# Kernel optimization log

Measured on AMD Instinct MI355X. Metric: run time of the kernel, lower is better.

## Reference

```python
import jax, jax.numpy as jnp
import numpy as np

N_NODES = 100000
N_EDGES = 800000
D_IN, D_H1, D_H2, D_OUT = 512, 256, 256, 64


def setup_inputs() -> dict:
    key = jax.random.key(0)
    ks = jax.random.split(key, 8)
    x = jax.random.normal(ks[0], (N_NODES, D_IN), dtype=jnp.float32)
    edge_index = jax.random.randint(ks[1], (2, N_EDGES), 0, N_NODES, dtype=jnp.int64)
    # Glorot-style scaled weights (PyG GCNConv uses glorot init; Linear uses kaiming-uniform).
    W1 = jax.random.normal(ks[2], (D_IN, D_H1), dtype=jnp.float32) / np.sqrt(D_IN)
    b1 = jnp.zeros((D_H1,), dtype=jnp.float32)
    W2 = jax.random.normal(ks[3], (D_H1, D_H2), dtype=jnp.float32) / np.sqrt(D_H1)
    b2 = jnp.zeros((D_H2,), dtype=jnp.float32)
    Wc = jax.random.normal(ks[4], (D_H2, D_OUT), dtype=jnp.float32) / np.sqrt(D_H2)
    bc = jnp.zeros((D_OUT,), dtype=jnp.float32)
    return {"x": x, "edge_index": edge_index, "W1": W1, "b1": b1,
            "W2": W2, "b2": b2, "Wc": Wc, "bc": bc}


def reference(x, edge_index, W1, b1, W2, b2, Wc, bc):
    # GCNModel.forward in eval mode (dropout is identity when training=False).
    N = x.shape[0]
    src, dst = edge_index[0], edge_index[1]
    # PyG GCNConv: add self-loops, symmetric normalization D^-1/2 (A+I) D^-1/2.
    deg = jnp.zeros((N,), x.dtype).at[dst].add(jnp.float32(1.0)) + 1.0  # in-degree + self-loop
    dinv = jax.lax.rsqrt(deg)                         # [N]
    norm = dinv[src] * dinv[dst]                      # [E] per-edge coefficient
    self_norm = (dinv * dinv)[:, None]                # [N,1] self-loop coefficient 1/deg

    def gcn_conv(h, W, b):
        h = h @ W                                     # transform first (PyG order)
        agg = jax.ops.segment_sum(h[src] * norm[:, None], dst, num_segments=N)
        return agg + h * self_norm + b

    h = jax.nn.relu(gcn_conv(x, W1, b1))
    h = jax.nn.relu(gcn_conv(h, W2, b2))
    return h @ Wc + bc                                # [N, num_classes]
```

## Files before the change

### kernel.cpp

```cpp
#include <hip/hip_runtime.h>
#include <cstdint>

#define DIN 512
#define DH  256
#define DOUT 64

typedef __attribute__((ext_vector_type(8))) short bf16x8;
typedef __attribute__((ext_vector_type(4))) float f32x4;
typedef unsigned int uint32;

__device__ __forceinline__ unsigned short f2bf(float f) {
    uint32 u = __float_as_uint(f);
    u += 0x7fff + ((u >> 16) & 1);
    return (unsigned short)(u >> 16);
}
__device__ __forceinline__ float bf2f(unsigned short h) {
    return __uint_as_float(((uint32)h) << 16);
}
__device__ __forceinline__ float bflo(uint32 u) { return __uint_as_float(u << 16); }
__device__ __forceinline__ float bfhi(uint32 u) { return __uint_as_float(u & 0xffff0000u); }

__global__ void detect_i64(const unsigned long long* ei, int n_check,
                           unsigned long long bound, int* flag) {
    __shared__ int ok;
    if (threadIdx.x == 0) ok = 1;
    __syncthreads();
    int bad = 0;
    for (int i = threadIdx.x; i < n_check; i += blockDim.x) {
        if (ei[i] >= bound) bad = 1;
    }
    if (bad) ok = 0;
    __syncthreads();
    if (threadIdx.x == 0) *flag = ok;
}

__device__ __forceinline__ int get_idx(const void* ei, int is64, int pos) {
    if (is64) return (int)((const long long*)ei)[pos];
    return ((const int*)ei)[pos];
}

__global__ void count_deg(const void* ei, const int* flag, int E, int* counts) {
    const int is64 = *flag;
    int e = blockIdx.x * blockDim.x + threadIdx.x;
    if (e >= E) return;
    int d = get_idx(ei, is64, E + e);
    atomicAdd(&counts[d], 1);
}

__global__ void compute_dinv(const int* counts, float* dinv, int N) {
    int i = blockIdx.x * blockDim.x + threadIdx.x;
    if (i < N) dinv[i] = rsqrtf((float)counts[i] + 1.0f);
}

#define SCAN_BLOCK 256
#define SCAN_ELEMS 1024

__global__ void scan1(const int* counts, int* out, int* blocksums, int N) {
    __shared__ int sh[SCAN_BLOCK];
    int base = blockIdx.x * SCAN_ELEMS;
    int t = threadIdx.x;
    int v[4];
    int s = 0;
    #pragma unroll
    for (int j = 0; j < 4; j++) {
        int idx = base + t * 4 + j;
        v[j] = (idx < N) ? counts[idx] : 0;
        s += v[j];
    }
    sh[t] = s;
    __syncthreads();
    for (int off = 1; off < SCAN_BLOCK; off <<= 1) {
        int x = (t >= off) ? sh[t - off] : 0;
        __syncthreads();
        sh[t] += x;
        __syncthreads();
    }
    int run = (t == 0) ? 0 : sh[t - 1];
    #pragma unroll
    for (int j = 0; j < 4; j++) {
        int idx = base + t * 4 + j;
        if (idx < N) out[idx] = run;
        run += v[j];
    }
    if (t == SCAN_BLOCK - 1) blocksums[blockIdx.x] = sh[t];
}

__global__ void scan2(int* blocksums, int NB) {
    __shared__ int sh[SCAN_BLOCK];
    int t = threadIdx.x;
    sh[t] = (t < NB) ? blocksums[t] : 0;
    __syncthreads();
    for (int off = 1; off < SCAN_BLOCK; off <<= 1) {
        int x = (t >= off) ? sh[t - off] : 0;
        __syncthreads();
        sh[t] += x;
        __syncthreads();
    }
    if (t < NB) blocksums[t] = (t == 0) ? 0 : sh[t - 1];
}

__global__ void scan3(int* row_ptr, const int* blocksums, int N, int E) {
    int i = blockIdx.x * blockDim.x + threadIdx.x;
    if (i < N) row_ptr[i] += blocksums[i / SCAN_ELEMS];
    if (i == N) row_ptr[N] = E;
}

__global__ void fill_csr(const void* ei, const int* flag, int E,
                         const int* row_ptr, int* cursor, int* col_idx,
                         const float* dinv, float* edge_w) {
    const int is64 = *flag;
    int e = blockIdx.x * blockDim.x + threadIdx.x;
    if (e >= E) return;
    int d = get_idx(ei, is64, E + e);
    int s = get_idx(ei, is64, e);
    int pos = row_ptr[d] + atomicAdd(&cursor[d], 1);
    col_idx[pos] = s;
    edge_w[pos] = dinv[s] * dinv[d];
}

__global__ void transpose_w(const float* __restrict__ W, unsigned short* __restrict__ Bt,
                            int K, int Nw) {
    int i = blockIdx.x * blockDim.x + threadIdx.x;
    if (i >= K * Nw) return;
    int k = i / Nw, n = i % Nw;
    Bt[(size_t)n * K + k] = f2bf(W[i]);
}

template <bool A_FP32>
__global__ __launch_bounds__(512) void gemm_mfma(const void* __restrict__ Ap,
                                                 const unsigned short* __restrict__ Bt,
                                                 unsigned short* __restrict__ C,
                                                 int M, int K) {
    __shared__ unsigned short lds[24576];
    unsigned short* As = lds;
    unsigned short* Bs = lds + 8192;
    const int tid = threadIdx.x;
    const int w = tid >> 6, l = tid & 63;
    const int m0 = blockIdx.x * 128;
    const int wr = w >> 2, wc = w & 3;

    f32x4 acc[4][4] = {};

    for (int k0 = 0; k0 < K; k0 += 64) {
        #pragma unroll
        for (int i = 0; i < 4; i++) {
            int row = i * 64 + (tid >> 3);
            const unsigned short* src = Bt + (size_t)row * K + k0 + (tid & 7) * 8;
            unsigned short* dst = Bs + row * 64 + (tid & 7) * 8;
            __builtin_amdgcn_global_load_lds(
                (const __attribute__((address_space(1))) uint32*)src,
                (__attribute__((address_space(3))) uint32*)dst, 16, 0, 0);
        }
        if (A_FP32) {
            const float* Af = (const float*)Ap;
            #pragma unroll
            for (int i = 0; i < 4; i++) {
                int row = i * 32 + (tid >> 4);
                int rg = m0 + row; if (rg > M - 1) rg = M - 1;
                int c4 = (tid & 15) * 4;
                float4 v = *(const float4*)(Af + (size_t)rg * K + k0 + c4);
                ushort4 h;
                h.x = f2bf(v.x); h.y = f2bf(v.y); h.z = f2bf(v.z); h.w = f2bf(v.w);
                *(ushort4*)(As + row * 64 + c4) = h;
            }
        } else {
            const unsigned short* Ab = (const unsigned short*)Ap;
            #pragma unroll
            for (int i = 0; i < 2; i++) {
                int row = i * 64 + (tid >> 3);
                int rg = m0 + row; if (rg > M - 1) rg = M - 1;
                const unsigned short* src = Ab + (size_t)rg * K + k0 + (tid & 7) * 8;
                unsigned short* dst = As + row * 64 + (tid & 7) * 8;
                __builtin_amdgcn_global_load_lds(
                    (const __attribute__((address_space(1))) uint32*)src,
                    (__attribute__((address_space(3))) uint32*)dst, 16, 0, 0);
            }
        }
        __syncthreads();
        #pragma unroll
        for (int ks = 0; ks < 2; ks++) {
            bf16x8 a[4], b[4];
            #pragma unroll
            for (int m = 0; m < 4; m++)
                a[m] = *(const bf16x8*)(As + (wr * 64 + m * 16 + (l & 15)) * 64 + ks * 32 + (l >> 4) * 8);
            #pragma unroll
            for (int n = 0; n < 4; n++)
                b[n] = *(const bf16x8*)(Bs + (wc * 64 + n * 16 + (l & 15)) * 64 + ks * 32 + (l >> 4) * 8);
            #pragma unroll
            for (int m = 0; m < 4; m++)
                #pragma unroll
                for (int n = 0; n < 4; n++)
                    acc[m][n] = __builtin_amdgcn_mfma_f32_16x16x32_bf16(a[m], b[n], acc[m][n], 0, 0, 0);
        }
        __syncthreads();
    }

    unsigned short* ep = lds + (w & 3) * 4096;
    #pragma unroll
    for (int ph = 0; ph < 2; ph++) {
        if ((w >> 2) == ph) {
            #pragma unroll
            for (int m = 0; m < 4; m++)
                #pragma unroll
                for (int n = 0; n < 4; n++)
                    #pragma unroll
                    for (int r = 0; r < 4; r++)
                        ep[(m * 16 + (l >> 4) * 4 + r) * 64 + n * 16 + (l & 15)] = f2bf(acc[m][n][r]);
        }
        __syncthreads();
        if ((w >> 2) == ph) {
            #pragma unroll
            for (int p = 0; p < 8; p++) {
                int row = p * 8 + (l >> 3);
                int gr = m0 + wr * 64 + row;
                uint4 v = *(const uint4*)(ep + row * 64 + (l & 7) * 8);
                if (gr < M)
                    *(uint4*)(C + (size_t)gr * 256 + wc * 64 + (l & 7) * 8) = v;
            }
        }
        __syncthreads();
    }
}

__global__ __launch_bounds__(256) void gemm_head(const unsigned short* __restrict__ A,
                                                 const unsigned short* __restrict__ Bt,
                                                 const float* __restrict__ bias,
                                                 float* __restrict__ out, int M) {
    __shared__ unsigned short As[128 * 64];
    __shared__ unsigned short Bs[64 * 64];
    const int tid = threadIdx.x;
    const int w = tid >> 6, l = tid & 63;
    const int m0 = blockIdx.x * 128;
    const int wr = w >> 1, wc = w & 1;
    f32x4 acc[4][2] = {};

    for (int k0 = 0; k0 < 256; k0 += 64) {
        #pragma unroll
        for (int i = 0; i < 4; i++) {
            int row = i * 32 + w * 8 + (l >> 3);
            int rg = m0 + row; if (rg > M - 1) rg = M - 1;
            __builtin_amdgcn_global_load_lds(
                (const __attribute__((address_space(1))) uint32*)(A + (size_t)rg * 256 + k0 + (l & 7) * 8),
                (__attribute__((address_space(3))) uint32*)(As + row * 64 + (l & 7) * 8), 16, 0, 0);
        }
        #pragma unroll
        for (int i = 0; i < 2; i++) {
            int row = i * 32 + w * 8 + (l >> 3);
            __builtin_amdgcn_global_load_lds(
                (const __attribute__((address_space(1))) uint32*)(Bt + (size_t)row * 256 + k0 + (l & 7) * 8),
                (__attribute__((address_space(3))) uint32*)(Bs + row * 64 + (l & 7) * 8), 16, 0, 0);
        }
        __syncthreads();
        #pragma unroll
        for (int ks = 0; ks < 2; ks++) {
            bf16x8 a[4], b[2];
            #pragma unroll
            for (int m = 0; m < 4; m++)
                a[m] = *(const bf16x8*)(As + (wr * 64 + m * 16 + (l & 15)) * 64 + ks * 32 + (l >> 4) * 8);
            #pragma unroll
            for (int n = 0; n < 2; n++)
                b[n] = *(const bf16x8*)(Bs + (wc * 32 + n * 16 + (l & 15)) * 64 + ks * 32 + (l >> 4) * 8);
            #pragma unroll
            for (int m = 0; m < 4; m++)
                #pragma unroll
                for (int n = 0; n < 2; n++)
                    acc[m][n] = __builtin_amdgcn_mfma_f32_16x16x32_bf16(a[m], b[n], acc[m][n], 0, 0, 0);
        }
        __syncthreads();
    }
    #pragma unroll
    for (int m = 0; m < 4; m++)
        #pragma unroll
        for (int n = 0; n < 2; n++)
            #pragma unroll
            for (int r = 0; r < 4; r++) {
                int gr = m0 + wr * 64 + m * 16 + (l >> 4) * 4 + r;
                int col = wc * 32 + n * 16 + (l & 15);
                if (gr < M) out[(size_t)gr * 64 + col] = acc[m][n][r] + bias[col];
            }
}

#define ACC8(v, wgt)                                    \
    do {                                                \
        acc[0] = fmaf(wgt, bflo(v.x), acc[0]);          \
        acc[1] = fmaf(wgt, bfhi(v.x), acc[1]);          \
        acc[2] = fmaf(wgt, bflo(v.y), acc[2]);          \
        acc[3] = fmaf(wgt, bfhi(v.y), acc[3]);          \
        acc[4] = fmaf(wgt, bflo(v.z), acc[4]);          \
        acc[5] = fmaf(wgt, bfhi(v.z), acc[5]);          \
        acc[6] = fmaf(wgt, bflo(v.w), acc[6]);          \
        acc[7] = fmaf(wgt, bfhi(v.w), acc[7]);          \
    } while (0)

__global__ __launch_bounds__(256) void aggregate_bf(const unsigned short* __restrict__ t,
                                                    const float* __restrict__ dinv,
                                                    const int* __restrict__ row_ptr,
                                                    const int* __restrict__ col_idx,
                                                    const float* __restrict__ edge_w,
                                                    const float* __restrict__ bias,
                                                    unsigned short* __restrict__ outb,
                                                    int N) {
    int wave = threadIdx.x >> 6;
    int lane = threadIdx.x & 63;
    int half = lane >> 5;
    int sl = lane & 31;
    int n = blockIdx.x * 8 + wave * 2 + half;
    if (n >= N) return;

    float dn = dinv[n];
    int r0 = row_ptr[n], r1 = row_ptr[n + 1];

    float acc[8];
    {
        uint4 sv = *(const uint4*)(t + (size_t)n * DH + sl * 8);
        float sn = dn * dn;
        acc[0] = bflo(sv.x) * sn; acc[1] = bfhi(sv.x) * sn;
        acc[2] = bflo(sv.y) * sn; acc[3] = bfhi(sv.y) * sn;
        acc[4] = bflo(sv.z) * sn; acc[5] = bfhi(sv.z) * sn;
        acc[6] = bflo(sv.w) * sn; acc[7] = bfhi(sv.w) * sn;
    }

    int j = r0;
    for (; j + 4 <= r1; j += 4) {
        int s0 = col_idx[j + 0], s1 = col_idx[j + 1];
        int s2 = col_idx[j + 2], s3 = col_idx[j + 3];
        float w0 = edge_w[j + 0], w1 = edge_w[j + 1];
        float w2 = edge_w[j + 2], w3 = edge_w[j + 3];
        uint4 v0 = *(const uint4*)(t + (size_t)s0 * DH + sl * 8);
        uint4 v1 = *(const uint4*)(t + (size_t)s1 * DH + sl * 8);
        uint4 v2 = *(const uint4*)(t + (size_t)s2 * DH + sl * 8);
        uint4 v3 = *(const uint4*)(t + (size_t)s3 * DH + sl * 8);
        ACC8(v0, w0); ACC8(v1, w1); ACC8(v2, w2); ACC8(v3, w3);
    }
    for (; j < r1; j++) {
        int s = col_idx[j];
        float wgt = edge_w[j];
        uint4 v = *(const uint4*)(t + (size_t)s * DH + sl * 8);
        ACC8(v, wgt);
    }

    float4 b0 = *(const float4*)(bias + sl * 8);
    float4 b1v = *(const float4*)(bias + sl * 8 + 4);
    acc[0] = fmaxf(acc[0] + b0.x, 0.f);  acc[1] = fmaxf(acc[1] + b0.y, 0.f);
    acc[2] = fmaxf(acc[2] + b0.z, 0.f);  acc[3] = fmaxf(acc[3] + b0.w, 0.f);
    acc[4] = fmaxf(acc[4] + b1v.x, 0.f); acc[5] = fmaxf(acc[5] + b1v.y, 0.f);
    acc[6] = fmaxf(acc[6] + b1v.z, 0.f); acc[7] = fmaxf(acc[7] + b1v.w, 0.f);

    uint4 o;
    o.x = (uint32)f2bf(acc[0]) | ((uint32)f2bf(acc[1]) << 16);
    o.y = (uint32)f2bf(acc[2]) | ((uint32)f2bf(acc[3]) << 16);
    o.z = (uint32)f2bf(acc[4]) | ((uint32)f2bf(acc[5]) << 16);
    o.w = (uint32)f2bf(acc[6]) | ((uint32)f2bf(acc[7]) << 16);
    *(uint4*)(outb + (size_t)n * DH + sl * 8) = o;
}

extern "C" void kernel_launch(void* const* d_in, const int* in_sizes, int n_in,
                              void* d_out, int out_size, void* d_ws, size_t ws_size,
                              hipStream_t stream) {
    const float* x  = (const float*)d_in[0];
    const void*  ei = d_in[1];
    const float* W1 = (const float*)d_in[2];
    const float* b1 = (const float*)d_in[3];
    const float* W2 = (const float*)d_in[4];
    const float* b2 = (const float*)d_in[5];
    const float* Wc = (const float*)d_in[6];
    const float* bc = (const float*)d_in[7];
    float* out = (float*)d_out;

    const int N = in_sizes[0] / DIN;
    const int E = in_sizes[1] / 2;

    char* ws = (char*)d_ws;
    size_t off = 0;
    auto alloc = [&](size_t bytes) -> void* {
        off = (off + 255) & ~(size_t)255;
        void* p = ws + off;
        off += bytes;
        return p;
    };

    int*   flag      = (int*)alloc(4);
    int*   counts    = (int*)alloc((size_t)N * 4);
    int*   row_ptr   = (int*)alloc((size_t)(N + 1) * 4);
    int*   col_idx   = (int*)alloc((size_t)E * 4);
    float* edge_w    = (float*)alloc((size_t)E * 4);
    int*   blocksums = (int*)alloc(1024 * 4);
    float* dinv      = (float*)alloc((size_t)N * 4);
    unsigned short* Bt1   = (unsigned short*)alloc((size_t)DH * DIN * 2);
    unsigned short* Bt2   = (unsigned short*)alloc((size_t)DH * DH * 2);
    unsigned short* Btc   = (unsigned short*)alloc((size_t)DOUT * DH * 2);
    unsigned short* t_buf = (unsigned short*)alloc((size_t)N * DH * 2);
    unsigned short* a_buf = (unsigned short*)alloc((size_t)N * DH * 2);

    const int NB = (N + SCAN_ELEMS - 1) / SCAN_ELEMS;
    const int gM = (N + 127) / 128;

    detect_i64<<<1, 256, 0, stream>>>((const unsigned long long*)ei, 1024,
                                      (unsigned long long)N, flag);
    transpose_w<<<(DIN * DH + 255) / 256, 256, 0, stream>>>(W1, Bt1, DIN, DH);
    transpose_w<<<(DH * DH + 255) / 256, 256, 0, stream>>>(W2, Bt2, DH, DH);
    transpose_w<<<(DH * DOUT + 255) / 256, 256, 0, stream>>>(Wc, Btc, DH, DOUT);

    hipMemsetAsync(counts, 0, (size_t)N * 4, stream);
    count_deg<<<(E + 255) / 256, 256, 0, stream>>>(ei, flag, E, counts);
    compute_dinv<<<(N + 255) / 256, 256, 0, stream>>>(counts, dinv, N);
    scan1<<<NB, SCAN_BLOCK, 0, stream>>>(counts, row_ptr, blocksums, N);
    scan2<<<1, SCAN_BLOCK, 0, stream>>>(blocksums, NB);
    scan3<<<(N + 1 + 255) / 256, 256, 0, stream>>>(row_ptr, blocksums, N, E);
    hipMemsetAsync(counts, 0, (size_t)N * 4, stream);
    fill_csr<<<(E + 255) / 256, 256, 0, stream>>>(ei, flag, E, row_ptr, counts, col_idx,
                                                  dinv, edge_w);

    gemm_mfma<true><<<gM, 512, 0, stream>>>(x, Bt1, t_buf, N, DIN);
    aggregate_bf<<<(N + 7) / 8, 256, 0, stream>>>(t_buf, dinv, row_ptr, col_idx, edge_w, b1, a_buf, N);
    gemm_mfma<false><<<gM, 512, 0, stream>>>(a_buf, Bt2, t_buf, N, DH);
    aggregate_bf<<<(N + 7) / 8, 256, 0, stream>>>(t_buf, dinv, row_ptr, col_idx, edge_w, b2, a_buf, N);
    gemm_head<<<gM, 256, 0, stream>>>(a_buf, Btc, bc, out, N);
}
```

Measured before the change: 411.2 us.

## Retile GEMM to 64-row blocks and XOR-swizzle LDS tiles to avoid bank conflicts

The main GEMM moves from 128-row tiles with 512 threads to 64-row tiles with 256 threads. Each wave now owns a 64-column slice of the full 256-wide output, which lets the epilogue run in a single phase. LDS tiles for A and B in both the main GEMM and the head GEMM are stored with an XOR swizzle on 16-byte groups to cut bank conflicts on the MFMA fragment reads. The fp32 A path now converts 8 floats per thread into one 16-byte store. The trade-off is that each block reuses B across only 64 rows, so B traffic per output row doubles, though more blocks are available for occupancy.

```diff
diff --git a/kernel.cpp b/kernel.cpp
--- a/kernel.cpp
+++ b/kernel.cpp
@@ -19,6 +19,9 @@
 }
 __device__ __forceinline__ float bflo(uint32 u) { return __uint_as_float(u << 16); }
 __device__ __forceinline__ float bfhi(uint32 u) { return __uint_as_float(u & 0xffff0000u); }
+__device__ __forceinline__ uint32 pk2(float lo, float hi) {
+    return (uint32)f2bf(lo) | ((uint32)f2bf(hi) << 16);
+}
 
 __global__ void detect_i64(const unsigned long long* ei, int n_check,
                            unsigned long long bound, int* flag) {
@@ -127,25 +130,25 @@
 }
 
 template <bool A_FP32>
-__global__ __launch_bounds__(512) void gemm_mfma(const void* __restrict__ Ap,
+__global__ __launch_bounds__(256) void gemm_mfma(const void* __restrict__ Ap,
                                                  const unsigned short* __restrict__ Bt,
                                                  unsigned short* __restrict__ C,
                                                  int M, int K) {
-    __shared__ unsigned short lds[24576];
+    __shared__ unsigned short lds[20480];
     unsigned short* As = lds;
-    unsigned short* Bs = lds + 8192;
+    unsigned short* Bs = lds + 4096;
     const int tid = threadIdx.x;
     const int w = tid >> 6, l = tid & 63;
-    const int m0 = blockIdx.x * 128;
-    const int wr = w >> 2, wc = w & 3;
+    const int m0 = blockIdx.x * 64;
 
     f32x4 acc[4][4] = {};
 
     for (int k0 = 0; k0 < K; k0 += 64) {
         #pragma unroll
-        for (int i = 0; i < 4; i++) {
-            int row = i * 64 + (tid >> 3);
-            const unsigned short* src = Bt + (size_t)row * K + k0 + (tid & 7) * 8;
+        for (int i = 0; i < 8; i++) {
+            int row = i * 32 + (tid >> 3);
+            int gq = (tid & 7) ^ (row & 7);
+            const unsigned short* src = Bt + (size_t)row * K + k0 + gq * 8;
             unsigned short* dst = Bs + row * 64 + (tid & 7) * 8;
             __builtin_amdgcn_global_load_lds(
                 (const __attribute__((address_space(1))) uint32*)src,
@@ -154,22 +157,26 @@
         if (A_FP32) {
             const float* Af = (const float*)Ap;
             #pragma unroll
-            for (int i = 0; i < 4; i++) {
-                int row = i * 32 + (tid >> 4);
+            for (int i = 0; i < 2; i++) {
+                int row = i * 32 + (tid >> 3);
+                int g = tid & 7;
                 int rg = m0 + row; if (rg > M - 1) rg = M - 1;
-                int c4 = (tid & 15) * 4;
-                float4 v = *(const float4*)(Af + (size_t)rg * K + k0 + c4);
-                ushort4 h;
-                h.x = f2bf(v.x); h.y = f2bf(v.y); h.z = f2bf(v.z); h.w = f2bf(v.w);
-                *(ushort4*)(As + row * 64 + c4) = h;
+                const float* s = Af + (size_t)rg * K + k0 + g * 8;
+                float4 v0 = *(const float4*)s;
+                float4 v1 = *(const float4*)(s + 4);
+                uint4 o;
+                o.x = pk2(v0.x, v0.y); o.y = pk2(v0.z, v0.w);
+                o.z = pk2(v1.x, v1.y); o.w = pk2(v1.z, v1.w);
+                *(uint4*)(As + row * 64 + ((g ^ (row & 7)) * 8)) = o;
             }
         } else {
             const unsigned short* Ab = (const unsigned short*)Ap;
             #pragma unroll
             for (int i = 0; i < 2; i++) {
-                int row = i * 64 + (tid >> 3);
+                int row = i * 32 + (tid >> 3);
+                int gq = (tid & 7) ^ (row & 7);
                 int rg = m0 + row; if (rg > M - 1) rg = M - 1;
-                const unsigned short* src = Ab + (size_t)rg * K + k0 + (tid & 7) * 8;
+                const unsigned short* src = Ab + (size_t)rg * K + k0 + gq * 8;
                 unsigned short* dst = As + row * 64 + (tid & 7) * 8;
                 __builtin_amdgcn_global_load_lds(
                     (const __attribute__((address_space(1))) uint32*)src,
@@ -181,11 +188,17 @@
         for (int ks = 0; ks < 2; ks++) {
             bf16x8 a[4], b[4];
             #pragma unroll
-            for (int m = 0; m < 4; m++)
-                a[m] = *(const bf16x8*)(As + (wr * 64 + m * 16 + (l & 15)) * 64 + ks * 32 + (l >> 4) * 8);
-            #pragma unroll
-            for (int n = 0; n < 4; n++)
-                b[n] = *(const bf16x8*)(Bs + (wc * 64 + n * 16 + (l & 15)) * 64 + ks * 32 + (l >> 4) * 8);
+            for (int m = 0; m < 4; m++) {
+                int arow = m * 16 + (l & 15);
+                int ag = (ks * 4 + (l >> 4)) ^ (arow & 7);
+                a[m] = *(const bf16x8*)(As + arow * 64 + ag * 8);
+            }
+            #pragma unroll
+            for (int n = 0; n < 4; n++) {
+                int brow = w * 64 + n * 16 + (l & 15);
+                int bg = (ks * 4 + (l >> 4)) ^ (brow & 7);
+                b[n] = *(const bf16x8*)(Bs + brow * 64 + bg * 8);
+            }
             #pragma unroll
             for (int m = 0; m < 4; m++)
                 #pragma unroll
@@ -195,30 +208,22 @@
         __syncthreads();
     }
 
-    unsigned short* ep = lds + (w & 3) * 4096;
+    unsigned short* ep = lds + w * 4096;
     #pragma unroll
-    for (int ph = 0; ph < 2; ph++) {
-        if ((w >> 2) == ph) {
-            #pragma unroll
-            for (int m = 0; m < 4; m++)
-                #pragma unroll
-                for (int n = 0; n < 4; n++)
-                    #pragma unroll
-                    for (int r = 0; r < 4; r++)
-                        ep[(m * 16 + (l >> 4) * 4 + r) * 64 + n * 16 + (l & 15)] = f2bf(acc[m][n][r]);
-        }
-        __syncthreads();
-        if ((w >> 2) == ph) {
-            #pragma unroll
-            for (int p = 0; p < 8; p++) {
-                int row = p * 8 + (l >> 3);
-                int gr = m0 + wr * 64 + row;
-                uint4 v = *(const uint4*)(ep + row * 64 + (l & 7) * 8);
-                if (gr < M)
-                    *(uint4*)(C + (size_t)gr * 256 + wc * 64 + (l & 7) * 8) = v;
-            }
-        }
-        __syncthreads();
+    for (int m = 0; m < 4; m++)
+        #pragma unroll
+        for (int n = 0; n < 4; n++)
+            #pragma unroll
+            for (int r = 0; r < 4; r++)
+                ep[(m * 16 + (l >> 4) * 4 + r) * 64 + n * 16 + (l & 15)] = f2bf(acc[m][n][r]);
+    __syncthreads();
+    #pragma unroll
+    for (int p = 0; p < 8; p++) {
+        int row = p * 8 + (l >> 3);
+        int gr = m0 + row;
+        uint4 v = *(const uint4*)(ep + row * 64 + (l & 7) * 8);
+        if (gr < M)
+            *(uint4*)(C + (size_t)gr * 256 + w * 64 + (l & 7) * 8) = v;
     }
 }
 
@@ -237,29 +242,37 @@
     for (int k0 = 0; k0 < 256; k0 += 64) {
         #pragma unroll
         for (int i = 0; i < 4; i++) {
-            int row = i * 32 + w * 8 + (l >> 3);
+            int row = i * 32 + (tid >> 3);
+            int gq = (tid & 7) ^ (row & 7);
             int rg = m0 + row; if (rg > M - 1) rg = M - 1;
             __builtin_amdgcn_global_load_lds(
-                (const __attribute__((address_space(1))) uint32*)(A + (size_t)rg * 256 + k0 + (l & 7) * 8),
-                (__attribute__((address_space(3))) uint32*)(As + row * 64 + (l & 7) * 8), 16, 0, 0);
+                (const __attribute__((address_space(1))) uint32*)(A + (size_t)rg * 256 + k0 + gq * 8),
+                (__attribute__((address_space(3))) uint32*)(As + row * 64 + (tid & 7) * 8), 16, 0, 0);
         }
         #pragma unroll
         for (int i = 0; i < 2; i++) {
-            int row = i * 32 + w * 8 + (l >> 3);
+            int row = i * 32 + (tid >> 3);
+            int gq = (tid & 7) ^ (row & 7);
             __builtin_amdgcn_global_load_lds(
-                (const __attribute__((address_space(1))) uint32*)(Bt + (size_t)row * 256 + k0 + (l & 7) * 8),
-                (__attribute__((address_space(3))) uint32*)(Bs + row * 64 + (l & 7) * 8), 16, 0, 0);
+                (const __attribute__((address_space(1))) uint32*)(Bt + (size_t)row * 256 + k0 + gq * 8),
+                (__attribute__((address_space(3))) uint32*)(Bs + row * 64 + (tid & 7) * 8), 16, 0, 0);
         }
         __syncthreads();
         #pragma unroll
         for (int ks = 0; ks < 2; ks++) {
             bf16x8 a[4], b[2];
             #pragma unroll
-            for (int m = 0; m < 4; m++)
-                a[m] = *(const bf16x8*)(As + (wr * 64 + m * 16 + (l & 15)) * 64 + ks * 32 + (l >> 4) * 8);
-            #pragma unroll
-            for (int n = 0; n < 2; n++)
-                b[n] = *(const bf16x8*)(Bs + (wc * 32 + n * 16 + (l & 15)) * 64 + ks * 32 + (l >> 4) * 8);
+            for (int m = 0; m < 4; m++) {
+                int arow = wr * 64 + m * 16 + (l & 15);
+                int ag = (ks * 4 + (l >> 4)) ^ (arow & 7);
+                a[m] = *(const bf16x8*)(As + arow * 64 + ag * 8);
+            }
+            #pragma unroll
+            for (int n = 0; n < 2; n++) {
+                int brow = wc * 32 + n * 16 + (l & 15);
+                int bg = (ks * 4 + (l >> 4)) ^ (brow & 7);
+                b[n] = *(const bf16x8*)(Bs + brow * 64 + bg * 8);
+            }
             #pragma unroll
             for (int m = 0; m < 4; m++)
                 #pragma unroll
@@ -347,10 +360,10 @@
     acc[6] = fmaxf(acc[6] + b1v.z, 0.f); acc[7] = fmaxf(acc[7] + b1v.w, 0.f);
 
     uint4 o;
-    o.x = (uint32)f2bf(acc[0]) | ((uint32)f2bf(acc[1]) << 16);
-    o.y = (uint32)f2bf(acc[2]) | ((uint32)f2bf(acc[3]) << 16);
-    o.z = (uint32)f2bf(acc[4]) | ((uint32)f2bf(acc[5]) << 16);
-    o.w = (uint32)f2bf(acc[6]) | ((uint32)f2bf(acc[7]) << 16);
+    o.x = pk2(acc[0], acc[1]);
+    o.y = pk2(acc[2], acc[3]);
+    o.z = pk2(acc[4], acc[5]);
+    o.w = pk2(acc[6], acc[7]);
     *(uint4*)(outb + (size_t)n * DH + sl * 8) = o;
 }
 
@@ -393,7 +406,8 @@
     unsigned short* a_buf = (unsigned short*)alloc((size_t)N * DH * 2);
 
     const int NB = (N + SCAN_ELEMS - 1) / SCAN_ELEMS;
-    const int gM = (N + 127) / 128;
+    const int gM64  = (N + 63) / 64;
+    const int gM128 = (N + 127) / 128;
 
     detect_i64<<<1, 256, 0, stream>>>((const unsigned long long*)ei, 1024,
                                       (unsigned long long)N, flag);
@@ -411,9 +425,9 @@
     fill_csr<<<(E + 255) / 256, 256, 0, stream>>>(ei, flag, E, row_ptr, counts, col_idx,
                                                   dinv, edge_w);
 
-    gemm_mfma<true><<<gM, 512, 0, stream>>>(x, Bt1, t_buf, N, DIN);
+    gemm_mfma<true><<<gM64, 256, 0, stream>>>(x, Bt1, t_buf, N, DIN);
     aggregate_bf<<<(N + 7) / 8, 256, 0, stream>>>(t_buf, dinv, row_ptr, col_idx, edge_w, b1, a_buf, N);
-    gemm_mfma<false><<<gM, 512, 0, stream>>>(a_buf, Bt2, t_buf, N, DH);
+    gemm_mfma<false><<<gM64, 256, 0, stream>>>(a_buf, Bt2, t_buf, N, DH);
     aggregate_bf<<<(N + 7) / 8, 256, 0, stream>>>(t_buf, dinv, row_ptr, col_idx, edge_w, b2, a_buf, N);
-    gemm_head<<<gM, 256, 0, stream>>>(a_buf, Btc, bc, out, N);
-}
+    gemm_head<<<gM128, 256, 0, stream>>>(a_buf, Btc, bc, out, N);
+}
```

After: 364.0 us. -11.5%, faster.
